# Kernel tuning notes

Measured on AMD Instinct MI355X. Metric: run time of the kernel, lower is better.

Reference implementation:

```python
import jax, jax.numpy as jnp
import numpy as np

N = 50000
E = 800000
DIM_IN = 128
DIM_H = 16
HEADS = 8
DIM_OUT = 16
NEG_SLOPE = 0.2


def setup_inputs() -> dict:
    key = jax.random.key(0)
    ks = jax.random.split(key, 12)
    def glorot(k, shape):
        fan_in = shape[0]
        return jax.random.normal(k, shape, dtype=jnp.float32) / np.sqrt(fan_in)
    x = jax.random.normal(ks[0], (N, DIM_IN), dtype=jnp.float32)
    edge_index = jax.random.randint(ks[1], (2, E), 0, N, dtype=jnp.int64)
    # layer 1: GATv2Conv(dim_in, dim_h, heads=8)
    Wl1 = glorot(ks[2], (DIM_IN, HEADS * DIM_H))
    Wr1 = glorot(ks[3], (DIM_IN, HEADS * DIM_H))
    att1 = glorot(ks[4], (HEADS, DIM_H))
    bias1 = jnp.zeros((HEADS * DIM_H,), dtype=jnp.float32)
    # layer 2: GATv2Conv(dim_h*heads, dim_out, heads=1)
    Wl2 = glorot(ks[5], (HEADS * DIM_H, DIM_OUT))
    Wr2 = glorot(ks[6], (HEADS * DIM_H, DIM_OUT))
    att2 = glorot(ks[7], (1, DIM_OUT))
    bias2 = jnp.zeros((DIM_OUT,), dtype=jnp.float32)
    return {"x": x, "edge_index": edge_index, "Wl1": Wl1, "Wr1": Wr1,
            "att1": att1, "bias1": bias1, "Wl2": Wl2, "Wr2": Wr2,
            "att2": att2, "bias2": bias2}


def gatv2_layer(x, src, dst, Wl, Wr, att, bias, n_nodes, heads, ch):
    # x: [N, F_in]; src/dst: [Etot] (self-loops included)
    xl = (x @ Wl).reshape(n_nodes, heads, ch)  # source transform
    xr = (x @ Wr).reshape(n_nodes, heads, ch)  # target transform
    e = jax.nn.leaky_relu(xl[src] + xr[dst], NEG_SLOPE)      # [Etot, H, C]
    logits = jnp.einsum('ehc,hc->eh', e, att)                # [Etot, H]
    # segment softmax over incoming edges of each target node
    m = jax.ops.segment_max(logits, dst, num_segments=n_nodes)
    a = jnp.exp(logits - m[dst])
    denom = jax.ops.segment_sum(a, dst, num_segments=n_nodes)
    alpha = a / denom[dst]                                   # [Etot, H]
    out = jax.ops.segment_sum(xl[src] * alpha[:, :, None], dst,
                              num_segments=n_nodes)          # [N, H, C]
    return out.reshape(n_nodes, heads * ch) + bias


def reference(x, edge_index, Wl1, Wr1, att1, bias1, Wl2, Wr2, att2, bias2):
    # PyG GATv2Conv adds self-loops by default
    loops = jnp.arange(N, dtype=edge_index.dtype)
    src = jnp.concatenate([edge_index[0], loops])
    dst = jnp.concatenate([edge_index[1], loops])
    # dropout is identity in eval mode
    h = gatv2_layer(x, src, dst, Wl1, Wr1, att1, bias1, N, HEADS, DIM_H)
    h = jax.nn.elu(h)
    h = gatv2_layer(h, src, dst, Wl2, Wr2, att2, bias2, N, 1, DIM_OUT)
    return h, jax.nn.log_softmax(h, axis=1)
```

## Files before the change

kernel.cpp:

```cpp
#include <hip/hip_runtime.h>
#include <hip/hip_bf16.h>
#include <hip/hip_fp16.h>
#include <math.h>

#define NN 50000
#define EE 800000
#define DIN 128
#define HEADS 8
#define DH 16
#define DOUT 16
#define NEG 0.2f
#define GM 32
#define GB ((NN + GM - 1) / GM)
#define NB ((NN + 255) / 256)
#define ABLK ((EE / 4 + 255) / 256)
#define NPART 8
#define RANGE (NN / NPART)
#define RB 1563
#define SCATB 64
#define BUCKCAP 110000
#define PAD 64

typedef __attribute__((ext_vector_type(8))) short bf16x8;
typedef __attribute__((ext_vector_type(4))) float f32x4;
typedef __attribute__((ext_vector_type(4))) int i32x4;
typedef _Float16 h16x2 __attribute__((ext_vector_type(2)));

__device__ __forceinline__ unsigned pack2bf(float a, float b) {
    union { __hip_bfloat162 h; unsigned u; } c;
    c.h = __float22bfloat162_rn(make_float2(a, b));
    return c.u;
}
__device__ __forceinline__ unsigned short f2bf(float v) {
    union { __hip_bfloat16 h; unsigned short u; } c;
    c.h = __float2bfloat16(v);
    return c.u;
}
__device__ __forceinline__ unsigned short f2h(float v) {
    union { __half h; unsigned short u; } c;
    c.h = __float2half(v);
    return c.u;
}
__device__ __forceinline__ h16x2 u2h(unsigned u) { union { unsigned u; h16x2 h; } c; c.u = u; return c.h; }
__device__ __forceinline__ unsigned h2u(h16x2 h) { union { h16x2 h; unsigned u; } c; c.h = h; return c.u; }
__device__ __forceinline__ float elu1(float x) { return x > 0.f ? x : __expf(x) - 1.f; }

__global__ __launch_bounds__(256) void init_bucket(int* __restrict__ cnt,
                                                   const float* __restrict__ Wl,
                                                   const float* __restrict__ Wr,
                                                   unsigned short* __restrict__ Wb,
                                                   const float* __restrict__ Wl2,
                                                   const float* __restrict__ Wr2,
                                                   unsigned short* __restrict__ Wb2,
                                                   const int* __restrict__ ei,
                                                   unsigned* __restrict__ bhead,
                                                   unsigned* __restrict__ bucket) {
    int b = blockIdx.x, t = threadIdx.x;
    if (b < NB) {
        int i = b * 256 + t;
        if (i < NN) cnt[i] = 1;
        return;
    } else if (b < NB + 128) {
        int i = (b - NB) * 256 + t;
        int n = i >> 7, k = i & 127;
        float v = (n < 128) ? Wl[k * 128 + n] : Wr[k * 128 + (n - 128)];
        Wb[i] = f2bf(v);
        return;
    } else if (b < NB + 144) {
        int i = (b - NB - 128) * 256 + t;
        int n = i >> 7, k = i & 127;
        float v = (n < 16) ? Wl2[k * 16 + n] : Wr2[k * 16 + (n - 16)];
        Wb2[i] = f2bf(v);
        return;
    }
    __shared__ unsigned lrec[1024];
    __shared__ unsigned lcnt[8], loff[8], lpos[8], gbase[8];
    int ab = b - (NB + 144);
    int i = ab * 256 + t;
    bool valid = i < EE / 4;
    i32x4 ss, dd;
    unsigned bb[4];
    if (valid) {
        ss = __builtin_nontemporal_load(((const i32x4*)ei) + i);
        dd = __builtin_nontemporal_load(((const i32x4*)(ei + EE)) + i);
    }
    if (t < 8) { lcnt[t] = 0; lpos[t] = 0; }
    __syncthreads();
    if (valid) {
#pragma unroll
        for (int e = 0; e < 4; ++e) {
            bb[e] = (unsigned)dd[e] / RANGE;
            atomicAdd(&lcnt[bb[e]], 1u);
        }
    }
    __syncthreads();
    if (t == 0) {
        unsigned run = 0;
#pragma unroll
        for (int q = 0; q < 8; ++q) { loff[q] = run; run += lcnt[q]; }
    }
    if (t < 8 && lcnt[t] > 0) gbase[t] = atomicAdd(&bhead[t], lcnt[t]);
    __syncthreads();
    if (valid) {
#pragma unroll
        for (int e = 0; e < 4; ++e) {
            unsigned p = atomicAdd(&lpos[bb[e]], 1u);
            lrec[loff[bb[e]] + p] = ((unsigned)ss[e] << 16) | (unsigned)dd[e];
        }
    }
    __syncthreads();
    unsigned total = loff[7] + lcnt[7];
    for (unsigned j = t; j < total; j += 256) {
        unsigned q = 0;
        while (q < 7 && j >= loff[q + 1]) ++q;
        bucket[(size_t)q * BUCKCAP + gbase[q] + (j - loff[q])] = lrec[j];
    }
}

__global__ __launch_bounds__(256) void scat_gemm1(const unsigned* __restrict__ bucket,
                                                  const unsigned* __restrict__ bhead,
                                                  int* __restrict__ cnt,
                                                  unsigned short* __restrict__ esrcPad,
                                                  const float* __restrict__ x,
                                                  const unsigned short* __restrict__ Wb,
                                                  unsigned short* __restrict__ xlb,
                                                  unsigned short* __restrict__ xr) {
    __shared__ unsigned short As[GM][136];
    __shared__ unsigned short Cs[GM][264];
    int t = threadIdx.x;
    if (blockIdx.x < NPART * SCATB) {
        int r = blockIdx.x & 7;
        int g = blockIdx.x >> 3;
        if (g == 0) {
            for (int dq = t; dq < RANGE; dq += 256) {
                int d = r * RANGE + dq;
                esrcPad[(unsigned)d * PAD] = (unsigned short)d;
            }
        }
        unsigned n = bhead[r];
        for (unsigned i = (unsigned)g * 256 + t; i < n; i += SCATB * 256) {
            unsigned rec = __builtin_nontemporal_load(bucket + (size_t)r * BUCKCAP + i);
            unsigned s = rec >> 16, d = rec & 0xffffu;
            int p = atomicAdd(&cnt[d], 1);
            esrcPad[d * PAD + p] = (unsigned short)s;
        }
        return;
    }
    int n0 = (blockIdx.x - NPART * SCATB) * GM;
    {
        int row = t >> 3, seg = t & 7;
        int nsrc = n0 + row < NN ? n0 + row : NN - 1;
        const f32x4* xp = (const f32x4*)(x + (size_t)nsrc * DIN + 16 * seg);
        f32x4 v0 = __builtin_nontemporal_load(xp);
        f32x4 v1 = __builtin_nontemporal_load(xp + 1);
        f32x4 v2 = __builtin_nontemporal_load(xp + 2);
        f32x4 v3 = __builtin_nontemporal_load(xp + 3);
        uint4 p0 = make_uint4(pack2bf(v0[0], v0[1]), pack2bf(v0[2], v0[3]),
                              pack2bf(v1[0], v1[1]), pack2bf(v1[2], v1[3]));
        uint4 p1 = make_uint4(pack2bf(v2[0], v2[1]), pack2bf(v2[2], v2[3]),
                              pack2bf(v3[0], v3[1]), pack2bf(v3[2], v3[3]));
        *(uint4*)&As[row][16 * seg]     = p0;
        *(uint4*)&As[row][16 * seg + 8] = p1;
    }
    __syncthreads();
    int lane = t & 63, w = t >> 6;
    int m = lane & 15, quad = lane >> 4;
    f32x4 acc[2][4];
#pragma unroll
    for (int mt = 0; mt < 2; ++mt)
#pragma unroll
        for (int nt = 0; nt < 4; ++nt) acc[mt][nt] = (f32x4){0.f, 0.f, 0.f, 0.f};
#pragma unroll
    for (int ks = 0; ks < 4; ++ks) {
        int k = 32 * ks + 8 * quad;
        bf16x8 a0 = *(const bf16x8*)&As[m][k];
        bf16x8 a1 = *(const bf16x8*)&As[16 + m][k];
#pragma unroll
        for (int nt = 0; nt < 4; ++nt) {
            int n = 64 * w + 16 * nt + m;
            bf16x8 b = *(const bf16x8*)(Wb + (size_t)n * 128 + k);
            acc[0][nt] = __builtin_amdgcn_mfma_f32_16x16x32_bf16(a0, b, acc[0][nt], 0, 0, 0);
            acc[1][nt] = __builtin_amdgcn_mfma_f32_16x16x32_bf16(a1, b, acc[1][nt], 0, 0, 0);
        }
    }
#pragma unroll
    for (int mt = 0; mt < 2; ++mt) {
#pragma unroll
        for (int nt = 0; nt < 4; ++nt) {
            int col = 64 * w + 16 * nt + m;
            int rbase = 16 * mt + 4 * quad;
#pragma unroll
            for (int r = 0; r < 4; ++r) Cs[rbase + r][col] = f2h(acc[mt][nt][r]);
        }
    }
    __syncthreads();
    {
        int row = t >> 3, seg = t & 7;
        int grow = n0 + row;
        if (grow < NN) {
            uint4 a0 = *(uint4*)&Cs[row][16 * seg];
            uint4 a1 = *(uint4*)&Cs[row][16 * seg + 8];
            *(uint4*)(xlb + (unsigned)grow * DIN + 16 * seg)     = a0;
            *(uint4*)(xlb + (unsigned)grow * DIN + 16 * seg + 8) = a1;
            uint4 b0 = *(uint4*)&Cs[row][128 + 16 * seg];
            uint4 b1 = *(uint4*)&Cs[row][128 + 16 * seg + 8];
            *(uint4*)(xr + (unsigned)grow * DIN + 16 * seg)     = b0;
            *(uint4*)(xr + (unsigned)grow * DIN + 16 * seg + 8) = b1;
        }
    }
}

__global__ __launch_bounds__(256) void l1_fused(const unsigned short* __restrict__ esrcPad,
                                                const int* __restrict__ cnt,
                                                const unsigned short* __restrict__ xlb,
                                                const unsigned short* __restrict__ xr,
                                                const float* __restrict__ att,
                                                const float* __restrict__ bias,
                                                unsigned short* __restrict__ hb) {
    int r = blockIdx.x & 7;
    int dq = (blockIdx.x >> 3) * 4 + (threadIdx.x >> 6);
    if (dq >= RANGE) return;
    int d = r * RANGE + dq;
    int lane = threadIdx.x & 63;
    int quarter = lane >> 4;
    int q16 = lane & 15;
    int rs = d * PAD;
    int re = rs + cnt[d];
    int last = re - 1;
    uint4 xru = ((const uint4*)(xr + (unsigned)d * DIN))[q16];
    h16x2 xh0 = u2h(xru.x), xh1 = u2h(xru.y), xh2 = u2h(xru.z), xh3 = u2h(xru.w);
    float4 at0 = ((const float4*)att)[2 * q16];
    float4 at1 = ((const float4*)att)[2 * q16 + 1];
    h16x2 ah0 = (h16x2){(_Float16)at0.x, (_Float16)at0.y};
    h16x2 ah1 = (h16x2){(_Float16)at0.z, (_Float16)at0.w};
    h16x2 ah2 = (h16x2){(_Float16)at1.x, (_Float16)at1.y};
    h16x2 ah3 = (h16x2){(_Float16)at1.z, (_Float16)at1.w};
    const h16x2 c06 = (h16x2){(_Float16)0.6f, (_Float16)0.6f};
    const h16x2 c04 = (h16x2){(_Float16)0.4f, (_Float16)0.4f};
    float4 a0 = make_float4(0.f, 0.f, 0.f, 0.f);
    float4 a1 = make_float4(0.f, 0.f, 0.f, 0.f);
    float l = 0.f;
    int slot = rs + quarter;
    int c0i = slot < last ? slot : last;
    unsigned s0 = esrcPad[c0i];
    int c1i = slot + 4 < last ? slot + 4 : last;
    unsigned s1 = esrcPad[c1i];
    uint4 row = ((const uint4*)(xlb + s0 * (unsigned)DIN))[q16];
    for (; slot < re; slot += 4) {
        uint4 cur = row;
        int c2i = slot + 8 < last ? slot + 8 : last;
        unsigned s2 = esrcPad[c2i];
        row = ((const uint4*)(xlb + s1 * (unsigned)DIN))[q16];
        s1 = s2;
        h16x2 c0 = u2h(cur.x), c1 = u2h(cur.y), c2 = u2h(cur.z), c3 = u2h(cur.w);
        h16x2 v0 = c0 + xh0, v1 = c1 + xh1, v2 = c2 + xh2, v3 = c3 + xh3;
        h16x2 w0 = v0 * c06 + u2h(h2u(v0) & 0x7fff7fffu) * c04;
        h16x2 w1 = v1 * c06 + u2h(h2u(v1) & 0x7fff7fffu) * c04;
        h16x2 w2 = v2 * c06 + u2h(h2u(v2) & 0x7fff7fffu) * c04;
        h16x2 w3 = v3 * c06 + u2h(h2u(v3) & 0x7fff7fffu) * c04;
        float w = __builtin_amdgcn_fdot2(w0, ah0, 0.f, false);
        w = __builtin_amdgcn_fdot2(w1, ah1, w, false);
        w = __builtin_amdgcn_fdot2(w2, ah2, w, false);
        w = __builtin_amdgcn_fdot2(w3, ah3, w, false);
        w += __shfl_xor(w, 1);
        float p = __expf(w);
        a0.x += p * (float)c0[0]; a0.y += p * (float)c0[1];
        a0.z += p * (float)c1[0]; a0.w += p * (float)c1[1];
        a1.x += p * (float)c2[0]; a1.y += p * (float)c2[1];
        a1.z += p * (float)c3[0]; a1.w += p * (float)c3[1];
        l += p;
    }
#pragma unroll
    for (int off = 16; off < 64; off <<= 1) {
        a0.x += __shfl_xor(a0.x, off); a0.y += __shfl_xor(a0.y, off);
        a0.z += __shfl_xor(a0.z, off); a0.w += __shfl_xor(a0.w, off);
        a1.x += __shfl_xor(a1.x, off); a1.y += __shfl_xor(a1.y, off);
        a1.z += __shfl_xor(a1.z, off); a1.w += __shfl_xor(a1.w, off);
        l += __shfl_xor(l, off);
    }
    if (quarter == 0) {
        float inv = 1.f / l;
        float4 b0 = ((const float4*)bias)[2 * q16];
        float4 b1 = ((const float4*)bias)[2 * q16 + 1];
        float4 o0, o1;
        o0.x = elu1(a0.x * inv + b0.x);
        o0.y = elu1(a0.y * inv + b0.y);
        o0.z = elu1(a0.z * inv + b0.z);
        o0.w = elu1(a0.w * inv + b0.w);
        o1.x = elu1(a1.x * inv + b1.x);
        o1.y = elu1(a1.y * inv + b1.y);
        o1.z = elu1(a1.z * inv + b1.z);
        o1.w = elu1(a1.w * inv + b1.w);
        uint4 pk = make_uint4(pack2bf(o0.x, o0.y), pack2bf(o0.z, o0.w),
                              pack2bf(o1.x, o1.y), pack2bf(o1.z, o1.w));
        ((uint4*)(hb + (unsigned)d * DIN))[q16] = pk;
    }
}

__global__ __launch_bounds__(256) void gemm2(const unsigned short* __restrict__ hb,
                                             const unsigned short* __restrict__ Wb2,
                                             float* __restrict__ xl2, float* __restrict__ xr2) {
    __shared__ unsigned short As[GM][136];
    int t = threadIdx.x;
    int n0 = blockIdx.x * GM;
    {
        int row = t >> 3, s8 = t & 7;
        int nsrc = n0 + row < NN ? n0 + row : NN - 1;
        const uint4* src = (const uint4*)(hb + (size_t)nsrc * DIN);
        *(uint4*)&As[row][8 * s8]      = src[s8];
        *(uint4*)&As[row][8 * s8 + 64] = src[s8 + 8];
    }
    __syncthreads();
    int lane = t & 63, w = t >> 6;
    int m = lane & 15, quad = lane >> 4;
    int mt = w & 1, nt = w >> 1;
    f32x4 acc = (f32x4){0.f, 0.f, 0.f, 0.f};
#pragma unroll
    for (int ks = 0; ks < 4; ++ks) {
        int k = 32 * ks + 8 * quad;
        bf16x8 a = *(const bf16x8*)&As[16 * mt + m][k];
        bf16x8 b = *(const bf16x8*)(Wb2 + (size_t)(16 * nt + m) * 128 + k);
        acc = __builtin_amdgcn_mfma_f32_16x16x32_bf16(a, b, acc, 0, 0, 0);
    }
    float* __restrict__ dst = (nt == 0) ? xl2 : xr2;
#pragma unroll
    for (int r = 0; r < 4; ++r) {
        int node = n0 + 16 * mt + 4 * quad + r;
        if (node < NN) dst[(size_t)node * DOUT + m] = acc[r];
    }
}

__global__ __launch_bounds__(256) void l2_fused(const unsigned short* __restrict__ esrcPad,
                                                const int* __restrict__ cnt,
                                                const float* __restrict__ xl,
                                                const float* __restrict__ xr,
                                                const float* __restrict__ att,
                                                const float* __restrict__ bias,
                                                float* __restrict__ out) {
    int r = blockIdx.x & 7;
    int dq = (blockIdx.x >> 3) * 4 + (threadIdx.x >> 6);
    if (dq >= RANGE) return;
    int d = r * RANGE + dq;
    int lane = threadIdx.x & 63;
    int sl = lane >> 2;
    int q = lane & 3;
    int rs = d * PAD;
    int re = rs + cnt[d];
    int last = re - 1;
    float4 xrq = ((const float4*)(xr + (unsigned)d * DOUT))[q];
    float4 atq = ((const float4*)att)[q];
    float4 acc = make_float4(0.f, 0.f, 0.f, 0.f);
    float l = 0.f;
    int slot = rs + sl;
    int c0 = slot < last ? slot : last;
    unsigned s0 = esrcPad[c0];
    for (; slot < re; slot += 16) {
        int c1 = slot + 16 < last ? slot + 16 : last;
        unsigned s1 = esrcPad[c1];
        float4 cur = ((const float4*)(xl + s0 * (unsigned)DOUT))[q];
        s0 = s1;
        float v0 = cur.x + xrq.x; v0 = fmaxf(v0, NEG * v0);
        float v1 = cur.y + xrq.y; v1 = fmaxf(v1, NEG * v1);
        float v2 = cur.z + xrq.z; v2 = fmaxf(v2, NEG * v2);
        float v3 = cur.w + xrq.w; v3 = fmaxf(v3, NEG * v3);
        float w = atq.x * v0 + atq.y * v1 + atq.z * v2 + atq.w * v3;
        w += __shfl_xor(w, 1);
        w += __shfl_xor(w, 2);
        float p = __expf(w);
        acc.x += p * cur.x; acc.y += p * cur.y;
        acc.z += p * cur.z; acc.w += p * cur.w;
        l += p;
    }
#pragma unroll
    for (int off = 4; off < 64; off <<= 1) {
        acc.x += __shfl_xor(acc.x, off);
        acc.y += __shfl_xor(acc.y, off);
        acc.z += __shfl_xor(acc.z, off);
        acc.w += __shfl_xor(acc.w, off);
        l += __shfl_xor(l, off);
    }
    float inv = 1.f / l;
    float4 b = ((const float4*)bias)[q];
    float4 v;
    v.x = acc.x * inv + b.x; v.y = acc.y * inv + b.y;
    v.z = acc.z * inv + b.z; v.w = acc.w * inv + b.w;
    float m = fmaxf(fmaxf(v.x, v.y), fmaxf(v.z, v.w));
    m = fmaxf(m, __shfl_xor(m, 1));
    m = fmaxf(m, __shfl_xor(m, 2));
    float es = __expf(v.x - m) + __expf(v.y - m) + __expf(v.z - m) + __expf(v.w - m);
    es += __shfl_xor(es, 1);
    es += __shfl_xor(es, 2);
    float lse = m + __logf(es);
    if (sl == 0) {
        ((float4*)(out + (size_t)d * DOUT))[q] = v;
        float4 ls;
        ls.x = v.x - lse; ls.y = v.y - lse; ls.z = v.z - lse; ls.w = v.w - lse;
        ((float4*)(out + (size_t)NN * DOUT + (size_t)d * DOUT))[q] = ls;
    }
}

extern "C" void kernel_launch(void* const* d_in, const int* in_sizes, int n_in,
                              void* d_out, int out_size, void* d_ws, size_t ws_size,
                              hipStream_t stream) {
    const float* x     = (const float*)d_in[0];
    const int*   ei    = (const int*)d_in[1];
    const float* Wl1   = (const float*)d_in[2];
    const float* Wr1   = (const float*)d_in[3];
    const float* att1  = (const float*)d_in[4];
    const float* bias1 = (const float*)d_in[5];
    const float* Wl2   = (const float*)d_in[6];
    const float* Wr2   = (const float*)d_in[7];
    const float* att2  = (const float*)d_in[8];
    const float* bias2 = (const float*)d_in[9];
    float* out = (float*)d_out;

    unsigned short* xr1 = (unsigned short*)d_ws;
    float* xl2    = (float*)(xr1 + (size_t)NN * DIN);
    float* xr2    = xl2 + (size_t)NN * DOUT;
    unsigned short* xlb = (unsigned short*)(xr2 + (size_t)NN * DOUT);
    unsigned short* hb  = xlb + (size_t)NN * DIN;
    unsigned short* Wb  = hb + (size_t)NN * DIN;
    unsigned short* Wb2 = Wb + 256 * 128;
    unsigned short* esrcPad = Wb2 + 32 * 128;
    int*   cnt    = (int*)(esrcPad + (size_t)NN * PAD);
    unsigned* bucket = (unsigned*)(cnt + NN);
    unsigned* bhead  = bucket + (size_t)8 * BUCKCAP;

    const int B = 256;
    hipMemsetAsync(bhead, 0, 8 * sizeof(unsigned), stream);
    init_bucket<<<NB + 144 + ABLK, B, 0, stream>>>(cnt, Wl1, Wr1, Wb, Wl2, Wr2, Wb2,
                                                   ei, bhead, bucket);
    scat_gemm1<<<NPART * SCATB + GB, B, 0, stream>>>(bucket, bhead, cnt, esrcPad,
                                                     x, Wb, xlb, xr1);
    l1_fused<<<NPART * RB, B, 0, stream>>>(esrcPad, cnt, xlb, xr1, att1, bias1, hb);
    gemm2<<<GB, B, 0, stream>>>(hb, Wb2, xl2, xr2);
    l2_fused<<<NPART * RB, B, 0, stream>>>(esrcPad, cnt, xl2, xr2, att2, bias2, out);
}
```

Before: 223.3 us.

## Fuse layer-2 linear transform into layer-1 aggregation epilogue

Removes the separate gemm2 kernel and the bf16 hidden-state buffer. Each wavefront in l1_fused now computes the ELU output in registers and multiplies it by fp32 Wl2/Wr2 using per-lane dot products and shuffle reductions, then writes xl2/xr2 directly. This saves a kernel launch and the write and read of the N×128 hidden tensor. In exchange every quarter-wave does eight extra reduction rounds of scalar fp32 FMAs instead of MFMA work, and weight reads are repeated per node.

```diff
diff --git a/kernel.cpp b/kernel.cpp
--- a/kernel.cpp
+++ b/kernel.cpp
@@ -51,7 +51,7 @@
                                                    unsigned short* __restrict__ Wb,
                                                    const float* __restrict__ Wl2,
                                                    const float* __restrict__ Wr2,
-                                                   unsigned short* __restrict__ Wb2,
+                                                   float* __restrict__ Wb2f,
                                                    const int* __restrict__ ei,
                                                    unsigned* __restrict__ bhead,
                                                    unsigned* __restrict__ bucket) {
@@ -70,7 +70,7 @@
         int i = (b - NB - 128) * 256 + t;
         int n = i >> 7, k = i & 127;
         float v = (n < 16) ? Wl2[k * 16 + n] : Wr2[k * 16 + (n - 16)];
-        Wb2[i] = f2bf(v);
+        Wb2f[i] = v;
         return;
     }
     __shared__ unsigned lrec[1024];
@@ -216,7 +216,9 @@
                                                 const unsigned short* __restrict__ xr,
                                                 const float* __restrict__ att,
                                                 const float* __restrict__ bias,
-                                                unsigned short* __restrict__ hb) {
+                                                const float* __restrict__ Wb2f,
+                                                float* __restrict__ xl2,
+                                                float* __restrict__ xr2) {
     int r = blockIdx.x & 7;
     int dq = (blockIdx.x >> 3) * 4 + (threadIdx.x >> 6);
     if (dq >= RANGE) return;
@@ -278,55 +280,33 @@
         a1.z += __shfl_xor(a1.z, off); a1.w += __shfl_xor(a1.w, off);
         l += __shfl_xor(l, off);
     }
-    if (quarter == 0) {
-        float inv = 1.f / l;
-        float4 b0 = ((const float4*)bias)[2 * q16];
-        float4 b1 = ((const float4*)bias)[2 * q16 + 1];
-        float4 o0, o1;
-        o0.x = elu1(a0.x * inv + b0.x);
-        o0.y = elu1(a0.y * inv + b0.y);
-        o0.z = elu1(a0.z * inv + b0.z);
-        o0.w = elu1(a0.w * inv + b0.w);
-        o1.x = elu1(a1.x * inv + b1.x);
-        o1.y = elu1(a1.y * inv + b1.y);
-        o1.z = elu1(a1.z * inv + b1.z);
-        o1.w = elu1(a1.w * inv + b1.w);
-        uint4 pk = make_uint4(pack2bf(o0.x, o0.y), pack2bf(o0.z, o0.w),
-                              pack2bf(o1.x, o1.y), pack2bf(o1.z, o1.w));
-        ((uint4*)(hb + (unsigned)d * DIN))[q16] = pk;
-    }
-}
-
-__global__ __launch_bounds__(256) void gemm2(const unsigned short* __restrict__ hb,
-                                             const unsigned short* __restrict__ Wb2,
-                                             float* __restrict__ xl2, float* __restrict__ xr2) {
-    __shared__ unsigned short As[GM][136];
-    int t = threadIdx.x;
-    int n0 = blockIdx.x * GM;
-    {
-        int row = t >> 3, s8 = t & 7;
-        int nsrc = n0 + row < NN ? n0 + row : NN - 1;
-        const uint4* src = (const uint4*)(hb + (size_t)nsrc * DIN);
-        *(uint4*)&As[row][8 * s8]      = src[s8];
-        *(uint4*)&As[row][8 * s8 + 64] = src[s8 + 8];
-    }
-    __syncthreads();
-    int lane = t & 63, w = t >> 6;
-    int m = lane & 15, quad = lane >> 4;
-    int mt = w & 1, nt = w >> 1;
-    f32x4 acc = (f32x4){0.f, 0.f, 0.f, 0.f};
-#pragma unroll
-    for (int ks = 0; ks < 4; ++ks) {
-        int k = 32 * ks + 8 * quad;
-        bf16x8 a = *(const bf16x8*)&As[16 * mt + m][k];
-        bf16x8 b = *(const bf16x8*)(Wb2 + (size_t)(16 * nt + m) * 128 + k);
-        acc = __builtin_amdgcn_mfma_f32_16x16x32_bf16(a, b, acc, 0, 0, 0);
-    }
-    float* __restrict__ dst = (nt == 0) ? xl2 : xr2;
-#pragma unroll
-    for (int r = 0; r < 4; ++r) {
-        int node = n0 + 16 * mt + 4 * quad + r;
-        if (node < NN) dst[(size_t)node * DOUT + m] = acc[r];
+    float inv = 1.f / l;
+    float4 b0 = ((const float4*)bias)[2 * q16];
+    float4 b1 = ((const float4*)bias)[2 * q16 + 1];
+    float o[8];
+    o[0] = elu1(a0.x * inv + b0.x);
+    o[1] = elu1(a0.y * inv + b0.y);
+    o[2] = elu1(a0.z * inv + b0.z);
+    o[3] = elu1(a0.w * inv + b0.w);
+    o[4] = elu1(a1.x * inv + b1.x);
+    o[5] = elu1(a1.y * inv + b1.y);
+    o[6] = elu1(a1.z * inv + b1.z);
+    o[7] = elu1(a1.w * inv + b1.w);
+#pragma unroll
+    for (int jj = 0; jj < 8; ++jj) {
+        int j = 8 * quarter + jj;
+        const f32x4* wp = (const f32x4*)(Wb2f + (unsigned)j * 128 + 8 * q16);
+        f32x4 w0 = wp[0], w1 = wp[1];
+        float p = o[0] * w0[0] + o[1] * w0[1] + o[2] * w0[2] + o[3] * w0[3]
+                + o[4] * w1[0] + o[5] * w1[1] + o[6] * w1[2] + o[7] * w1[3];
+        p += __shfl_xor(p, 1);
+        p += __shfl_xor(p, 2);
+        p += __shfl_xor(p, 4);
+        p += __shfl_xor(p, 8);
+        if (q16 == jj) {
+            if (j < 16) xl2[(unsigned)d * DOUT + j] = p;
+            else        xr2[(unsigned)d * DOUT + (j - 16)] = p;
+        }
     }
 }
 
@@ -418,21 +398,20 @@
     float* xl2    = (float*)(xr1 + (size_t)NN * DIN);
     float* xr2    = xl2 + (size_t)NN * DOUT;
     unsigned short* xlb = (unsigned short*)(xr2 + (size_t)NN * DOUT);
-    unsigned short* hb  = xlb + (size_t)NN * DIN;
-    unsigned short* Wb  = hb + (size_t)NN * DIN;
-    unsigned short* Wb2 = Wb + 256 * 128;
-    unsigned short* esrcPad = Wb2 + 32 * 128;
+    unsigned short* Wb  = xlb + (size_t)NN * DIN;
+    float* Wb2f   = (float*)(Wb + 256 * 128);
+    unsigned short* esrcPad = (unsigned short*)(Wb2f + 32 * 128);
     int*   cnt    = (int*)(esrcPad + (size_t)NN * PAD);
     unsigned* bucket = (unsigned*)(cnt + NN);
     unsigned* bhead  = bucket + (size_t)8 * BUCKCAP;
 
     const int B = 256;
     hipMemsetAsync(bhead, 0, 8 * sizeof(unsigned), stream);
-    init_bucket<<<NB + 144 + ABLK, B, 0, stream>>>(cnt, Wl1, Wr1, Wb, Wl2, Wr2, Wb2,
+    init_bucket<<<NB + 144 + ABLK, B, 0, stream>>>(cnt, Wl1, Wr1, Wb, Wl2, Wr2, Wb2f,
                                                    ei, bhead, bucket);
     scat_gemm1<<<NPART * SCATB + GB, B, 0, stream>>>(bucket, bhead, cnt, esrcPad,
                                                      x, Wb, xlb, xr1);
-    l1_fused<<<NPART * RB, B, 0, stream>>>(esrcPad, cnt, xlb, xr1, att1, bias1, hb);
-    gemm2<<<GB, B, 0, stream>>>(hb, Wb2, xl2, xr2);
+    l1_fused<<<NPART * RB, B, 0, stream>>>(esrcPad, cnt, xlb, xr1, att1, bias1,
+                                           Wb2f, xl2, xr2);
     l2_fused<<<NPART * RB, B, 0, stream>>>(esrcPad, cnt, xl2, xr2, att2, bias2, out);
 }
```

New measurement: 236.8 us. 1.06x slower.
